# Performance work log

Hardware: AMD Instinct MI355X
Metric: run time of the kernel (lower is better)

Reference implementation:

```python
import jax, jax.numpy as jnp
import numpy as np

B, S, DM, H = 2, 2048, 512, 8
DH = DM // H


def setup_inputs() -> dict:
    key = jax.random.key(0)
    ks = jax.random.split(key, 20)
    sc = 0.02
    d = {}
    d["q"] = jax.random.normal(ks[0], (B, S, DM), jnp.float32)
    d["k"] = jax.random.normal(ks[1], (B, S, DM), jnp.float32)
    d["v"] = jax.random.normal(ks[2], (B, S, DM), jnp.float32)
    d["xdiff"] = jax.random.normal(ks[3], (B, S, S), jnp.float32)
    d["mask"] = jax.random.randint(ks[4], (B, 1, 1, S), 0, 2, jnp.int32)
    # learned params (keras Dense: kernel + bias)
    d["Wq"] = jax.random.normal(ks[5], (DM, DM), jnp.float32) * sc
    d["bq"] = jnp.zeros((DM,), jnp.float32)
    d["Wk"] = jax.random.normal(ks[6], (DM, DM), jnp.float32) * sc
    d["bk"] = jnp.zeros((DM,), jnp.float32)
    d["Wv"] = jax.random.normal(ks[7], (DM, DM), jnp.float32) * sc
    d["bv"] = jnp.zeros((DM,), jnp.float32)
    d["Wa"] = jax.random.normal(ks[8], (DM, H), jnp.float32) * sc
    d["ba"] = jnp.zeros((H,), jnp.float32)
    d["Wb"] = jax.random.normal(ks[9], (DM, H), jnp.float32) * sc
    d["bb"] = jnp.zeros((H,), jnp.float32)
    d["Wo"] = jax.random.normal(ks[10], (DM, DM), jnp.float32) * sc
    d["bo"] = jnp.zeros((DM,), jnp.float32)
    return d


def reference(q, k, v, xdiff, mask, Wq, bq, Wk, bk, Wv, bv, Wa, ba, Wb, bb, Wo, bo):
    b, s, dm = q.shape
    h, dh = H, DH
    qp = q @ Wq + bq            # [B,S,DM]
    kp = k @ Wk + bk
    vp = v @ Wv + bv
    # per-head alpha/beta from projected q: [B,S,H] -> [B,H,S]
    a = jnp.transpose(qp @ Wa + ba, (0, 2, 1))
    bb_ = jnp.transpose(qp @ Wb + bb, (0, 2, 1))
    # split heads -> [B,H,S,DH]
    qh = qp.reshape(b, s, h, dh).transpose(0, 2, 1, 3)
    kh = kp.reshape(b, s, h, dh).transpose(0, 2, 1, 3)
    vh = vp.reshape(b, s, h, dh).transpose(0, 2, 1, 3)
    logits = jnp.einsum('bhqd,bhkd->bhqk', qh, kh) / jnp.sqrt(jnp.float32(dh))
    logits = logits + mask.astype(jnp.float32) * (-1e9)
    xd = xdiff[:, None]          # [B,1,S,S] broadcast over heads
    logits = logits + a[..., None] * xd + bb_[..., None] * (xd * xd)
    attn = jax.nn.softmax(logits, axis=-1)
    out = jnp.einsum('bhqk,bhkd->bhqd', attn, vh)
    out = out.transpose(0, 2, 1, 3).reshape(b, s, dm)
    return out @ Wo + bo, attn
```

## Files before the change

kernel.cpp:

```cpp
#include <hip/hip_runtime.h>
#include <stdint.h>

#define BB 2
#define SS 2048
#define DMODEL 512
#define NH 8
#define DHD 64

typedef __attribute__((ext_vector_type(8))) short bf16x8;
typedef __attribute__((ext_vector_type(4))) short s16x4;
typedef __attribute__((ext_vector_type(4))) float fx4;

__device__ __forceinline__ short f2bf(float f) {
    union { float f; uint32_t u; } c; c.f = f;
    uint32_t u = c.u;
    u += 0x7fffu + ((u >> 16) & 1u);
    return (short)(u >> 16);
}
__device__ __forceinline__ float bf2f(short s) {
    union { uint32_t u; float f; } c; c.u = ((uint32_t)(uint16_t)s) << 16;
    return c.f;
}

template<int A_BF16, int OUT_BF16>
__global__ __launch_bounds__(256, 4) void gemm_bias_k(
    const void* __restrict__ Ap, const float* __restrict__ W,
    const float* __restrict__ bias, void* __restrict__ Cp)
{
    __shared__ short As[64 * 40];
    __shared__ short Bs[64 * 40];
    const int tid = threadIdx.x;
    const int w = tid >> 6, lane = tid & 63;
    const int cl = lane & 15, quad = lane >> 4;
    const int mi = w >> 1, ni = w & 1;
    const int m0 = blockIdx.x * 64, n0 = blockIdx.y * 64;
    const float* Af = (const float*)Ap;
    const short* Ab = (const short*)Ap;
    fx4 acc[2][2] = {};

    for (int k0 = 0; k0 < DMODEL; k0 += 32) {
#pragma unroll
        for (int it = 0; it < 2; ++it) {
            int idx = tid + it * 256;
            int row = idx >> 3, kq = (idx & 7) * 4;
            s16x4 sv;
            if (A_BF16) {
                sv = *(const s16x4*)&Ab[(size_t)(m0 + row) * DMODEL + k0 + kq];
            } else {
                const float4 vv = *(const float4*)&Af[(size_t)(m0 + row) * DMODEL + k0 + kq];
                sv.x = f2bf(vv.x); sv.y = f2bf(vv.y); sv.z = f2bf(vv.z); sv.w = f2bf(vv.w);
            }
            *(s16x4*)&As[row * 40 + kq] = sv;
        }
#pragma unroll
        for (int it = 0; it < 2; ++it) {
            int idx = tid + it * 256;
            int kk = idx >> 4, nq = (idx & 15) * 4;
            const float4 vv = *(const float4*)&W[(size_t)(k0 + kk) * DMODEL + n0 + nq];
            Bs[(nq + 0) * 40 + kk] = f2bf(vv.x);
            Bs[(nq + 1) * 40 + kk] = f2bf(vv.y);
            Bs[(nq + 2) * 40 + kk] = f2bf(vv.z);
            Bs[(nq + 3) * 40 + kk] = f2bf(vv.w);
        }
        __syncthreads();
        bf16x8 af[2], bfr[2];
#pragma unroll
        for (int i = 0; i < 2; ++i)
            af[i] = *(const bf16x8*)&As[(mi * 32 + i * 16 + cl) * 40 + quad * 8];
#pragma unroll
        for (int j = 0; j < 2; ++j)
            bfr[j] = *(const bf16x8*)&Bs[(ni * 32 + j * 16 + cl) * 40 + quad * 8];
#pragma unroll
        for (int i = 0; i < 2; ++i)
#pragma unroll
            for (int j = 0; j < 2; ++j)
                acc[i][j] = __builtin_amdgcn_mfma_f32_16x16x32_bf16(af[i], bfr[j], acc[i][j], 0, 0, 0);
        __syncthreads();
    }
#pragma unroll
    for (int i = 0; i < 2; ++i) {
#pragma unroll
        for (int j = 0; j < 2; ++j) {
            int col = n0 + ni * 32 + j * 16 + cl;
            float bv = bias[col];
#pragma unroll
            for (int r = 0; r < 4; ++r) {
                int row = m0 + mi * 32 + i * 16 + quad * 4 + r;
                float v = acc[i][j][r] + bv;
                if (OUT_BF16) ((short*)Cp)[(size_t)row * DMODEL + col] = f2bf(v);
                else          ((float*)Cp)[(size_t)row * DMODEL + col] = v;
            }
        }
    }
}

__global__ __launch_bounds__(64) void ab_k(
    const short* __restrict__ qp,
    const float* __restrict__ Wa, const float* __restrict__ ba,
    const float* __restrict__ Wb, const float* __restrict__ bbias,
    float* __restrict__ a_ws, float* __restrict__ b_ws)
{
    const int r = blockIdx.x;
    const int b = r >> 11, s = r & 2047;
    const int lane = threadIdx.x;
    float qv[8];
    s16x4 q0 = *(const s16x4*)&qp[(size_t)r * DMODEL + lane * 8];
    s16x4 q1 = *(const s16x4*)&qp[(size_t)r * DMODEL + lane * 8 + 4];
    qv[0] = bf2f(q0.x); qv[1] = bf2f(q0.y); qv[2] = bf2f(q0.z); qv[3] = bf2f(q0.w);
    qv[4] = bf2f(q1.x); qv[5] = bf2f(q1.y); qv[6] = bf2f(q1.z); qv[7] = bf2f(q1.w);
    float pa[8] = {}, pb[8] = {};
#pragma unroll
    for (int kk = 0; kk < 8; ++kk) {
        int k = lane * 8 + kk;
        const float4 wa0 = *(const float4*)&Wa[k * 8];
        const float4 wa1 = *(const float4*)&Wa[k * 8 + 4];
        const float4 wb0 = *(const float4*)&Wb[k * 8];
        const float4 wb1 = *(const float4*)&Wb[k * 8 + 4];
        float qk = qv[kk];
        pa[0] += qk * wa0.x; pa[1] += qk * wa0.y; pa[2] += qk * wa0.z; pa[3] += qk * wa0.w;
        pa[4] += qk * wa1.x; pa[5] += qk * wa1.y; pa[6] += qk * wa1.z; pa[7] += qk * wa1.w;
        pb[0] += qk * wb0.x; pb[1] += qk * wb0.y; pb[2] += qk * wb0.z; pb[3] += qk * wb0.w;
        pb[4] += qk * wb1.x; pb[5] += qk * wb1.y; pb[6] += qk * wb1.z; pb[7] += qk * wb1.w;
    }
#pragma unroll
    for (int h = 0; h < 8; ++h) {
#pragma unroll
        for (int off = 1; off < 64; off <<= 1) {
            pa[h] += __shfl_xor(pa[h], off);
            pb[h] += __shfl_xor(pb[h], off);
        }
    }
    if (lane == 0) {
#pragma unroll
        for (int h = 0; h < 8; ++h) {
            a_ws[(b * NH + h) * SS + s] = pa[h] + ba[h];
            b_ws[(b * NH + h) * SS + s] = pb[h] + bbias[h];
        }
    }
}

__global__ __launch_bounds__(256, 2) void attn_k(
    const short* __restrict__ qp, const short* __restrict__ kp, const short* __restrict__ vp,
    const float* __restrict__ a_ws, const float* __restrict__ b_ws,
    const float* __restrict__ xdiff, const int* __restrict__ mask,
    float* __restrict__ attn, short* __restrict__ ao)
{
    __shared__ short qs[16 * 72];
    __shared__ short kv[4][64 * 72];
    __shared__ short ps[4][16 * 72];
    __shared__ float redm[64], reds[64], rowa[16], rowb[16];

    const int tid = threadIdx.x;
    const int w = tid >> 6, lane = tid & 63;
    const int cl = lane & 15, quad = lane >> 4;
    const int bh = blockIdx.x;
    const int b = bh >> 3, h = bh & 7;
    const int q0 = blockIdx.y * 16;
    const int bS = b * SS;

    for (int idx = tid; idx < 16 * 64; idx += 256) {
        int i = idx >> 6, k = idx & 63;
        qs[i * 72 + k] = qp[(size_t)(bS + q0 + i) * DMODEL + h * DHD + k];
    }
    if (tid < 16) {
        rowa[tid] = a_ws[(b * NH + h) * SS + q0 + tid];
        rowb[tid] = b_ws[(b * NH + h) * SS + q0 + tid];
    }
    __syncthreads();

    bf16x8 qf[2];
#pragma unroll
    for (int kc = 0; kc < 2; ++kc)
        qf[kc] = *(const bf16x8*)&qs[cl * 72 + kc * 32 + quad * 8];
    float ra[4], rb[4];
#pragma unroll
    for (int r = 0; r < 4; ++r) { ra[r] = rowa[quad * 4 + r]; rb[r] = rowb[quad * 4 + r]; }

    short* kvw = kv[w];
    short* psw = ps[w];
    const int j0w = w * 512;

    fx4 s[8][4];
    float rmax[4] = {-3e38f, -3e38f, -3e38f, -3e38f};

#pragma unroll
    for (int t = 0; t < 8; ++t) {
        const int j0 = j0w + t * 64;
#pragma unroll
        for (int p = 0; p < 16; ++p) {
            int jr = quad + p * 4;
            *(s16x4*)&kvw[jr * 72 + cl * 4] =
                *(const s16x4*)&kp[(size_t)(bS + j0 + jr) * DMODEL + h * DHD + cl * 4];
        }
        fx4 qk[4] = {};
#pragma unroll
        for (int nb = 0; nb < 4; ++nb)
#pragma unroll
            for (int kc = 0; kc < 2; ++kc) {
                bf16x8 kf = *(const bf16x8*)&kvw[(nb * 16 + cl) * 72 + kc * 32 + quad * 8];
                qk[nb] = __builtin_amdgcn_mfma_f32_16x16x32_bf16(qf[kc], kf, qk[nb], 0, 0, 0);
            }
#pragma unroll
        for (int nb = 0; nb < 4; ++nb) {
            const int j = j0 + nb * 16 + cl;
            const float mv = -1.0e9f * (float)mask[bS + j];
#pragma unroll
            for (int r = 0; r < 4; ++r) {
                const int qi = q0 + quad * 4 + r;
                const float xd = xdiff[(size_t)(bS + qi) * SS + j];
                float v = qk[nb][r] * 0.125f + mv + ra[r] * xd + rb[r] * (xd * xd);
                s[t][nb][r] = v;
                rmax[r] = fmaxf(rmax[r], v);
            }
        }
    }

#pragma unroll
    for (int off = 1; off < 16; off <<= 1)
#pragma unroll
        for (int r = 0; r < 4; ++r)
            rmax[r] = fmaxf(rmax[r], __shfl_xor(rmax[r], off));
    if (cl == 0)
#pragma unroll
        for (int r = 0; r < 4; ++r) redm[w * 16 + quad * 4 + r] = rmax[r];
    __syncthreads();
    float gm[4];
#pragma unroll
    for (int r = 0; r < 4; ++r) {
        int i = quad * 4 + r;
        gm[r] = fmaxf(fmaxf(redm[i], redm[16 + i]), fmaxf(redm[32 + i], redm[48 + i]));
    }

    float rsum[4] = {};
#pragma unroll
    for (int t = 0; t < 8; ++t)
#pragma unroll
        for (int nb = 0; nb < 4; ++nb)
#pragma unroll
            for (int r = 0; r < 4; ++r) {
                float e = exp2f((s[t][nb][r] - gm[r]) * 1.44269504f);
                s[t][nb][r] = e;
                rsum[r] += e;
            }
#pragma unroll
    for (int off = 1; off < 16; off <<= 1)
#pragma unroll
        for (int r = 0; r < 4; ++r)
            rsum[r] += __shfl_xor(rsum[r], off);
    if (cl == 0)
#pragma unroll
        for (int r = 0; r < 4; ++r) reds[w * 16 + quad * 4 + r] = rsum[r];
    __syncthreads();
    float gs[4];
#pragma unroll
    for (int r = 0; r < 4; ++r) {
        int i = quad * 4 + r;
        gs[r] = 1.0f / (reds[i] + reds[16 + i] + reds[32 + i] + reds[48 + i]);
    }

    fx4 oacc[4] = {};
    float* attn_bh = attn + (size_t)(b * NH + h) * SS * SS;
#pragma unroll
    for (int t = 0; t < 8; ++t) {
        const int j0 = j0w + t * 64;
#pragma unroll
        for (int p4 = 0; p4 < 16; ++p4) {
            s16x4 tmp;
            tmp.x = vp[(size_t)(bS + j0 + p4 * 4 + 0) * DMODEL + h * DHD + lane];
            tmp.y = vp[(size_t)(bS + j0 + p4 * 4 + 1) * DMODEL + h * DHD + lane];
            tmp.z = vp[(size_t)(bS + j0 + p4 * 4 + 2) * DMODEL + h * DHD + lane];
            tmp.w = vp[(size_t)(bS + j0 + p4 * 4 + 3) * DMODEL + h * DHD + lane];
            *(s16x4*)&kvw[lane * 72 + p4 * 4] = tmp;
        }
#pragma unroll
        for (int nb = 0; nb < 4; ++nb) {
            const int j = j0 + nb * 16 + cl;
#pragma unroll
            for (int r = 0; r < 4; ++r) {
                float p = s[t][nb][r] * gs[r];
                attn_bh[(size_t)(q0 + quad * 4 + r) * SS + j] = p;
                psw[(quad * 4 + r) * 72 + nb * 16 + cl] = f2bf(p);
            }
        }
        bf16x8 pf[2];
#pragma unroll
        for (int kc = 0; kc < 2; ++kc)
            pf[kc] = *(const bf16x8*)&psw[cl * 72 + kc * 32 + quad * 8];
#pragma unroll
        for (int nb = 0; nb < 4; ++nb)
#pragma unroll
            for (int kc = 0; kc < 2; ++kc) {
                bf16x8 vf = *(const bf16x8*)&kvw[(nb * 16 + cl) * 72 + kc * 32 + quad * 8];
                oacc[nb] = __builtin_amdgcn_mfma_f32_16x16x32_bf16(pf[kc], vf, oacc[nb], 0, 0, 0);
            }
    }

    __syncthreads();
    float* ored = (float*)kv;
#pragma unroll
    for (int nb = 0; nb < 4; ++nb)
#pragma unroll
        for (int r = 0; r < 4; ++r)
            ored[w * 1024 + (quad * 4 + r) * 64 + nb * 16 + cl] = oacc[nb][r];
    __syncthreads();
    {
        int i = tid >> 4, dq = (tid & 15) * 4;
        float sx = 0, sy = 0, sz = 0, sw = 0;
#pragma unroll
        for (int ww = 0; ww < 4; ++ww) {
            const float4 vv = *(const float4*)&ored[ww * 1024 + i * 64 + dq];
            sx += vv.x; sy += vv.y; sz += vv.z; sw += vv.w;
        }
        s16x4 o;
        o.x = f2bf(sx); o.y = f2bf(sy); o.z = f2bf(sz); o.w = f2bf(sw);
        *(s16x4*)&ao[(size_t)(bS + q0 + i) * DMODEL + h * DHD + dq] = o;
    }
}

extern "C" void kernel_launch(void* const* d_in, const int* in_sizes, int n_in,
                              void* d_out, int out_size, void* d_ws, size_t ws_size,
                              hipStream_t stream)
{
    (void)in_sizes; (void)n_in; (void)out_size; (void)ws_size;
    const float* q     = (const float*)d_in[0];
    const float* k     = (const float*)d_in[1];
    const float* v     = (const float*)d_in[2];
    const float* xdiff = (const float*)d_in[3];
    const int*   mask  = (const int*)d_in[4];
    const float* Wq = (const float*)d_in[5];
    const float* bq = (const float*)d_in[6];
    const float* Wk = (const float*)d_in[7];
    const float* bk = (const float*)d_in[8];
    const float* Wv = (const float*)d_in[9];
    const float* bv = (const float*)d_in[10];
    const float* Wa = (const float*)d_in[11];
    const float* ba = (const float*)d_in[12];
    const float* Wb = (const float*)d_in[13];
    const float* bb = (const float*)d_in[14];
    const float* Wo = (const float*)d_in[15];
    const float* bo = (const float*)d_in[16];

    char* ws = (char*)d_ws;
    short* qp   = (short*)(ws + 0);
    short* kp   = (short*)(ws + 4194304);
    short* vp   = (short*)(ws + 8388608);
    float* a_ws = (float*)(ws + 12582912);
    float* b_ws = (float*)(ws + 12713984);
    short* ao   = (short*)(ws + 12845056);

    float* out  = (float*)d_out;
    float* attn = out + (size_t)BB * SS * DMODEL;

    dim3 g(64, 8), blk(256);
    hipLaunchKernelGGL((gemm_bias_k<0, 1>), g, blk, 0, stream, q, Wq, bq, qp);
    hipLaunchKernelGGL((gemm_bias_k<0, 1>), g, blk, 0, stream, k, Wk, bk, kp);
    hipLaunchKernelGGL((gemm_bias_k<0, 1>), g, blk, 0, stream, v, Wv, bv, vp);
    hipLaunchKernelGGL(ab_k, dim3(4096), dim3(64), 0, stream, qp, Wa, ba, Wb, bb, a_ws, b_ws);
    hipLaunchKernelGGL(attn_k, dim3(16, 128), dim3(256), 0, stream,
                       qp, kp, vp, a_ws, b_ws, xdiff, mask, attn, ao);
    hipLaunchKernelGGL((gemm_bias_k<1, 0>), g, blk, 0, stream, ao, Wo, bo, out);
}
```

Measured before the change: 547.0 us.

## Transpose V in projection, read K/V fragments directly, widen attention blocks with XCD-aware mapping

The V projection now writes V transposed per head, so the attention kernel can load V MFMA fragments straight from global memory. K fragments are also read directly, which removes the LDS staging of K and V. The attention block grows to 8 waves, each covering 256 keys, and block indices are remapped so query tiles are grouped per XCD. The log2e factor is folded into the scale, mask and alpha/beta coefficients, attn is written with nontemporal stores, and MFMA sections get raised wave priority. The trade-off is uncoalesced global fragment loads and an extra cross-wave reduction step.

```diff
diff --git a/kernel.cpp b/kernel.cpp
--- a/kernel.cpp
+++ b/kernel.cpp
@@ -22,7 +22,7 @@
     return c.f;
 }
 
-template<int A_BF16, int OUT_BF16>
+template<int A_BF16, int OUT_MODE>
 __global__ __launch_bounds__(256, 4) void gemm_bias_k(
     const void* __restrict__ Ap, const float* __restrict__ W,
     const float* __restrict__ bias, void* __restrict__ Cp)
@@ -83,12 +83,23 @@
         for (int j = 0; j < 2; ++j) {
             int col = n0 + ni * 32 + j * 16 + cl;
             float bv = bias[col];
-#pragma unroll
-            for (int r = 0; r < 4; ++r) {
-                int row = m0 + mi * 32 + i * 16 + quad * 4 + r;
-                float v = acc[i][j][r] + bv;
-                if (OUT_BF16) ((short*)Cp)[(size_t)row * DMODEL + col] = f2bf(v);
-                else          ((float*)Cp)[(size_t)row * DMODEL + col] = v;
+            if (OUT_MODE == 2) {
+                int row0 = m0 + mi * 32 + i * 16 + quad * 4;
+                int bb_ = row0 >> 11, sr = row0 & (SS - 1);
+                s16x4 o;
+                o.x = f2bf(acc[i][j][0] + bv);
+                o.y = f2bf(acc[i][j][1] + bv);
+                o.z = f2bf(acc[i][j][2] + bv);
+                o.w = f2bf(acc[i][j][3] + bv);
+                *(s16x4*)&((short*)Cp)[((size_t)(bb_ * DMODEL + col)) * SS + sr] = o;
+            } else {
+#pragma unroll
+                for (int r = 0; r < 4; ++r) {
+                    int row = m0 + mi * 32 + i * 16 + quad * 4 + r;
+                    float v = acc[i][j][r] + bv;
+                    if (OUT_MODE == 1) ((short*)Cp)[(size_t)row * DMODEL + col] = f2bf(v);
+                    else               ((float*)Cp)[(size_t)row * DMODEL + col] = v;
+                }
             }
         }
     }
@@ -139,76 +150,68 @@
     }
 }
 
-__global__ __launch_bounds__(256, 2) void attn_k(
-    const short* __restrict__ qp, const short* __restrict__ kp, const short* __restrict__ vp,
+__global__ __launch_bounds__(512, 4) void attn_k(
+    const short* __restrict__ qp, const short* __restrict__ kp, const short* __restrict__ vT,
     const float* __restrict__ a_ws, const float* __restrict__ b_ws,
     const float* __restrict__ xdiff, const int* __restrict__ mask,
     float* __restrict__ attn, short* __restrict__ ao)
 {
-    __shared__ short qs[16 * 72];
-    __shared__ short kv[4][64 * 72];
-    __shared__ short ps[4][16 * 72];
-    __shared__ float redm[64], reds[64], rowa[16], rowb[16];
+    __shared__ char smem[32768];
+    __shared__ float redm[128], reds[128];
 
     const int tid = threadIdx.x;
     const int w = tid >> 6, lane = tid & 63;
     const int cl = lane & 15, quad = lane >> 4;
-    const int bh = blockIdx.x;
-    const int b = bh >> 3, h = bh & 7;
-    const int q0 = blockIdx.y * 16;
+
+    const int wg = blockIdx.x;
+    const int sp = wg >> 3, xcd = wg & 7;
+    const int h = sp & 7;
+    const int bqt = xcd * 32 + (sp >> 3);
+    const int b = bqt >> 7, qt = bqt & 127;
+    const int q0 = qt * 16;
     const int bS = b * SS;
 
-    for (int idx = tid; idx < 16 * 64; idx += 256) {
-        int i = idx >> 6, k = idx & 63;
-        qs[i * 72 + k] = qp[(size_t)(bS + q0 + i) * DMODEL + h * DHD + k];
-    }
-    if (tid < 16) {
-        rowa[tid] = a_ws[(b * NH + h) * SS + q0 + tid];
-        rowb[tid] = b_ws[(b * NH + h) * SS + q0 + tid];
-    }
-    __syncthreads();
+    const float LOG2E = 1.44269504f;
 
     bf16x8 qf[2];
 #pragma unroll
     for (int kc = 0; kc < 2; ++kc)
-        qf[kc] = *(const bf16x8*)&qs[cl * 72 + kc * 32 + quad * 8];
+        qf[kc] = *(const bf16x8*)&qp[(size_t)(bS + q0 + cl) * DMODEL + h * DHD + kc * 32 + quad * 8];
+
     float ra[4], rb[4];
 #pragma unroll
-    for (int r = 0; r < 4; ++r) { ra[r] = rowa[quad * 4 + r]; rb[r] = rowb[quad * 4 + r]; }
-
-    short* kvw = kv[w];
-    short* psw = ps[w];
-    const int j0w = w * 512;
-
-    fx4 s[8][4];
+    for (int r = 0; r < 4; ++r) {
+        int qi = q0 + quad * 4 + r;
+        ra[r] = a_ws[(b * NH + h) * SS + qi] * LOG2E;
+        rb[r] = b_ws[(b * NH + h) * SS + qi] * LOG2E;
+    }
+
+    const int j0w = w * 256;
+    fx4 s[4][4];
     float rmax[4] = {-3e38f, -3e38f, -3e38f, -3e38f};
 
 #pragma unroll
-    for (int t = 0; t < 8; ++t) {
+    for (int t = 0; t < 4; ++t) {
         const int j0 = j0w + t * 64;
-#pragma unroll
-        for (int p = 0; p < 16; ++p) {
-            int jr = quad + p * 4;
-            *(s16x4*)&kvw[jr * 72 + cl * 4] =
-                *(const s16x4*)&kp[(size_t)(bS + j0 + jr) * DMODEL + h * DHD + cl * 4];
-        }
         fx4 qk[4] = {};
+        __builtin_amdgcn_s_setprio(1);
 #pragma unroll
         for (int nb = 0; nb < 4; ++nb)
 #pragma unroll
             for (int kc = 0; kc < 2; ++kc) {
-                bf16x8 kf = *(const bf16x8*)&kvw[(nb * 16 + cl) * 72 + kc * 32 + quad * 8];
+                bf16x8 kf = *(const bf16x8*)&kp[(size_t)(bS + j0 + nb * 16 + cl) * DMODEL + h * DHD + kc * 32 + quad * 8];
                 qk[nb] = __builtin_amdgcn_mfma_f32_16x16x32_bf16(qf[kc], kf, qk[nb], 0, 0, 0);
             }
+        __builtin_amdgcn_s_setprio(0);
 #pragma unroll
         for (int nb = 0; nb < 4; ++nb) {
             const int j = j0 + nb * 16 + cl;
-            const float mv = -1.0e9f * (float)mask[bS + j];
+            const float mv = -1.442695e9f * (float)mask[bS + j];
 #pragma unroll
             for (int r = 0; r < 4; ++r) {
                 const int qi = q0 + quad * 4 + r;
                 const float xd = xdiff[(size_t)(bS + qi) * SS + j];
-                float v = qk[nb][r] * 0.125f + mv + ra[r] * xd + rb[r] * (xd * xd);
+                float v = qk[nb][r] * 0.18033688f + mv + ra[r] * xd + rb[r] * (xd * xd);
                 s[t][nb][r] = v;
                 rmax[r] = fmaxf(rmax[r], v);
             }
@@ -228,17 +231,21 @@
 #pragma unroll
     for (int r = 0; r < 4; ++r) {
         int i = quad * 4 + r;
-        gm[r] = fmaxf(fmaxf(redm[i], redm[16 + i]), fmaxf(redm[32 + i], redm[48 + i]));
+        float m0_ = fmaxf(redm[i],      redm[16 + i]);
+        float m1_ = fmaxf(redm[32 + i], redm[48 + i]);
+        float m2_ = fmaxf(redm[64 + i], redm[80 + i]);
+        float m3_ = fmaxf(redm[96 + i], redm[112 + i]);
+        gm[r] = fmaxf(fmaxf(m0_, m1_), fmaxf(m2_, m3_));
     }
 
     float rsum[4] = {};
 #pragma unroll
-    for (int t = 0; t < 8; ++t)
+    for (int t = 0; t < 4; ++t)
 #pragma unroll
         for (int nb = 0; nb < 4; ++nb)
 #pragma unroll
             for (int r = 0; r < 4; ++r) {
-                float e = exp2f((s[t][nb][r] - gm[r]) * 1.44269504f);
+                float e = exp2f(s[t][nb][r] - gm[r]);
                 s[t][nb][r] = e;
                 rsum[r] += e;
             }
@@ -255,30 +262,25 @@
 #pragma unroll
     for (int r = 0; r < 4; ++r) {
         int i = quad * 4 + r;
-        gs[r] = 1.0f / (reds[i] + reds[16 + i] + reds[32 + i] + reds[48 + i]);
+        float t0 = reds[i]      + reds[16 + i] + reds[32 + i] + reds[48 + i];
+        float t1 = reds[64 + i] + reds[80 + i] + reds[96 + i] + reds[112 + i];
+        gs[r] = 1.0f / (t0 + t1);
     }
 
     fx4 oacc[4] = {};
     float* attn_bh = attn + (size_t)(b * NH + h) * SS * SS;
-#pragma unroll
-    for (int t = 0; t < 8; ++t) {
+    short* psw = (short*)smem + w * (16 * 72);
+    const size_t vbase = (size_t)((b * NH + h) * DHD) * SS;
+#pragma unroll
+    for (int t = 0; t < 4; ++t) {
         const int j0 = j0w + t * 64;
-#pragma unroll
-        for (int p4 = 0; p4 < 16; ++p4) {
-            s16x4 tmp;
-            tmp.x = vp[(size_t)(bS + j0 + p4 * 4 + 0) * DMODEL + h * DHD + lane];
-            tmp.y = vp[(size_t)(bS + j0 + p4 * 4 + 1) * DMODEL + h * DHD + lane];
-            tmp.z = vp[(size_t)(bS + j0 + p4 * 4 + 2) * DMODEL + h * DHD + lane];
-            tmp.w = vp[(size_t)(bS + j0 + p4 * 4 + 3) * DMODEL + h * DHD + lane];
-            *(s16x4*)&kvw[lane * 72 + p4 * 4] = tmp;
-        }
 #pragma unroll
         for (int nb = 0; nb < 4; ++nb) {
             const int j = j0 + nb * 16 + cl;
 #pragma unroll
             for (int r = 0; r < 4; ++r) {
                 float p = s[t][nb][r] * gs[r];
-                attn_bh[(size_t)(q0 + quad * 4 + r) * SS + j] = p;
+                __builtin_nontemporal_store(p, &attn_bh[(size_t)(q0 + quad * 4 + r) * SS + j]);
                 psw[(quad * 4 + r) * 72 + nb * 16 + cl] = f2bf(p);
             }
         }
@@ -286,28 +288,30 @@
 #pragma unroll
         for (int kc = 0; kc < 2; ++kc)
             pf[kc] = *(const bf16x8*)&psw[cl * 72 + kc * 32 + quad * 8];
+        __builtin_amdgcn_s_setprio(1);
 #pragma unroll
         for (int nb = 0; nb < 4; ++nb)
 #pragma unroll
             for (int kc = 0; kc < 2; ++kc) {
-                bf16x8 vf = *(const bf16x8*)&kvw[(nb * 16 + cl) * 72 + kc * 32 + quad * 8];
+                bf16x8 vf = *(const bf16x8*)&vT[vbase + (size_t)(nb * 16 + cl) * SS + j0 + kc * 32 + quad * 8];
                 oacc[nb] = __builtin_amdgcn_mfma_f32_16x16x32_bf16(pf[kc], vf, oacc[nb], 0, 0, 0);
             }
+        __builtin_amdgcn_s_setprio(0);
     }
 
     __syncthreads();
-    float* ored = (float*)kv;
+    float* ored = (float*)smem;
 #pragma unroll
     for (int nb = 0; nb < 4; ++nb)
 #pragma unroll
         for (int r = 0; r < 4; ++r)
             ored[w * 1024 + (quad * 4 + r) * 64 + nb * 16 + cl] = oacc[nb][r];
     __syncthreads();
-    {
+    if (tid < 256) {
         int i = tid >> 4, dq = (tid & 15) * 4;
         float sx = 0, sy = 0, sz = 0, sw = 0;
 #pragma unroll
-        for (int ww = 0; ww < 4; ++ww) {
+        for (int ww = 0; ww < 8; ++ww) {
             const float4 vv = *(const float4*)&ored[ww * 1024 + i * 64 + dq];
             sx += vv.x; sy += vv.y; sz += vv.z; sw += vv.w;
         }
@@ -343,7 +347,7 @@
     char* ws = (char*)d_ws;
     short* qp   = (short*)(ws + 0);
     short* kp   = (short*)(ws + 4194304);
-    short* vp   = (short*)(ws + 8388608);
+    short* vT   = (short*)(ws + 8388608);
     float* a_ws = (float*)(ws + 12582912);
     float* b_ws = (float*)(ws + 12713984);
     short* ao   = (short*)(ws + 12845056);
@@ -354,9 +358,9 @@
     dim3 g(64, 8), blk(256);
     hipLaunchKernelGGL((gemm_bias_k<0, 1>), g, blk, 0, stream, q, Wq, bq, qp);
     hipLaunchKernelGGL((gemm_bias_k<0, 1>), g, blk, 0, stream, k, Wk, bk, kp);
-    hipLaunchKernelGGL((gemm_bias_k<0, 1>), g, blk, 0, stream, v, Wv, bv, vp);
+    hipLaunchKernelGGL((gemm_bias_k<0, 2>), g, blk, 0, stream, v, Wv, bv, vT);
     hipLaunchKernelGGL(ab_k, dim3(4096), dim3(64), 0, stream, qp, Wa, ba, Wb, bb, a_ws, b_ws);
-    hipLaunchKernelGGL(attn_k, dim3(16, 128), dim3(256), 0, stream,
-                       qp, kp, vp, a_ws, b_ws, xdiff, mask, attn, ao);
+    hipLaunchKernelGGL(attn_k, dim3(2048), dim3(512), 0, stream,
+                       qp, kp, vT, a_ws, b_ws, xdiff, mask, attn, ao);
     hipLaunchKernelGGL((gemm_bias_k<1, 0>), g, blk, 0, stream, ao, Wo, bo, out);
 }
```

Result: slower. 560.8 us (+2.5%).
